# Kernel tuning notes

Hardware: AMD Instinct MI355X
Metric: run time of the kernel (lower is better)

Reference implementation:

```python
import jax, jax.numpy as jnp
import numpy as np

GAMMA = 2.0
NUM_CLASSES = 33

def _cdist(x):
    # pairwise euclidean distance per batch: x [B,N,C] -> [B,N,N]
    sq = jnp.sum(x * x, axis=-1)                      # [B,N]
    d2 = sq[:, :, None] + sq[:, None, :] - 2.0 * jnp.einsum('bnc,bmc->bnm', x, x)
    d2 = jnp.maximum(d2, 0.0)
    d = jnp.sqrt(jnp.where(d2 > 0, d2, 1.0))          # safe sqrt (zero-distance -> 0, no nan grad)
    return jnp.where(d2 > 0, d, 0.0)


def setup_inputs() -> dict:
    key = jax.random.key(0)
    k1, k2, k3 = jax.random.split(key, 3)
    B, N, C = 2, 4096, NUM_CLASSES
    predictions = jax.random.normal(k1, (B, N, C), dtype=jnp.float32)
    targets = jax.random.randint(k2, (B, N), 0, C, dtype=jnp.int32)
    y_ohe = jax.nn.one_hot(targets, C, dtype=jnp.float32)
    pred_choice = jax.random.randint(k3, (B, N), 0, C, dtype=jnp.int32)
    return {"predictions": predictions, "y_ohe": y_ohe, "targets": targets, "pred_choice": pred_choice}


def reference(predictions, y_ohe, targets, pred_choice):
    B, N, C = predictions.shape
    # cross-entropy (mean over all B*N positions, no class weights)
    logp = jax.nn.log_softmax(predictions, axis=-1)                       # [B,N,C]
    logp_t = jnp.take_along_axis(logp, targets[..., None].astype(jnp.int32), axis=-1)[..., 0]
    ce_loss = -jnp.mean(logp_t)                                           # scalar

    # distance-map KL term
    dis_map = _cdist(y_ohe)                                               # [B,N,N]
    dis_map = jnp.where(dis_map > 1.0, 0.9, dis_map)
    dis_map = jnp.where(dis_map < 1.0, 0.05, dis_map)
    pred_prob = jax.nn.softmax(predictions, axis=-1)
    pred_map = _cdist(pred_prob)                                          # [B,N,N]
    # torch F.kl_div(input, target) with default 'mean': mean(target*(log(target)-input))
    dis_map_loss = jnp.mean(dis_map * (jnp.log(dis_map) - pred_map))

    # focal weighting of the (scalar) CE loss
    pn = jnp.take_along_axis(jnp.exp(logp), targets[..., None].astype(jnp.int32), axis=-1)[..., 0]
    pn = pn.reshape(-1)                                                   # [B*N]
    loss = jnp.mean((1.0 - pn) ** GAMMA * ce_loss)

    # dice loss: per-class loop collapses exactly to a global match count
    eps = 1.0
    matches = jnp.sum((targets.reshape(-1) == pred_choice.reshape(-1)).astype(jnp.float32))
    total = targets.size
    dice = 1.0 - 2.0 * ((matches + eps) / (2.0 * total + eps))

    return loss + dice + dis_map_loss
```

## Files before the change

kernel.cpp:

```cpp
#include <hip/hip_runtime.h>
#include <math.h>

#define BB 2
#define NN 4096
#define CC 33
#define RP 40
#define TILE 64
#define NTILES (NN / TILE)
#define NJT 3
#define NPB 715
#define ROWBLK 256
#define PAIRBLK (BB * NPB)
#define NSLOT 64
#define SLOTSTR 32

#define AS1 __attribute__((address_space(1)))
#define AS3 __attribute__((address_space(3)))

typedef __attribute__((ext_vector_type(8))) short frag_ab;
typedef __attribute__((ext_vector_type(4))) float f32x4;

__device__ __forceinline__ float fast_sqrt(float x) {
    return __builtin_amdgcn_sqrtf(x);
}
__device__ __forceinline__ unsigned f2bf(float x) {
    unsigned u = __float_as_uint(x);
    return (u + 0x7FFFu + ((u >> 16) & 1u)) >> 16;
}
__device__ __forceinline__ float bf2f(unsigned b) {
    return __uint_as_float(b << 16);
}

__global__ __launch_bounds__(256) void row_kernel(
    const float* __restrict__ pred, const int* __restrict__ targets,
    const int* __restrict__ pred_choice, unsigned short* __restrict__ p16,
    float2* __restrict__ part_row, int* __restrict__ part_match,
    float* __restrict__ slotf, unsigned* __restrict__ subcnt,
    unsigned* __restrict__ master)
{
    __shared__ __align__(16) float sraw[32 * CC];
    __shared__ float2 lds_cf[4];
    __shared__ int lds_mt[4];

    if (blockIdx.x == 0) {
        for (int i = threadIdx.x; i < NSLOT * SLOTSTR; i += 256) {
            slotf[i] = 0.0f;
            subcnt[i] = 0u;
        }
        if (threadIdx.x == 0) *master = 0u;
    }

    int l = threadIdx.x & 63;
    int w = threadIdx.x >> 6;

    {
        const float4* src = (const float4*)(pred + (size_t)blockIdx.x * 32 * CC);
        __builtin_amdgcn_global_load_lds(
            (const AS1 void*)(src + w * 64 + l),
            (AS3 void*)((char*)sraw + w * 1024), 16, 0, 0);
        if (threadIdx.x < 8) {
            float4 tv = src[256 + threadIdx.x];
            ((float4*)sraw)[256 + threadIdx.x] = tv;
        }
    }
    __syncthreads();

    int r = l >> 3;
    int c = l & 7;
    int rloc = w * 8 + r;
    int row = blockIdx.x * 32 + rloc;

    float v[4];
    #pragma unroll
    for (int k = 0; k < 4; k++) v[k] = sraw[rloc * CC + 4 * c + k];
    float v32 = sraw[rloc * CC + 32];

    float m = fmaxf(fmaxf(v[0], v[1]), fmaxf(v[2], v[3]));
    if (c == 0) m = fmaxf(m, v32);
    m = fmaxf(m, __shfl_xor(m, 1));
    m = fmaxf(m, __shfl_xor(m, 2));
    m = fmaxf(m, __shfl_xor(m, 4));

    float e[4];
    float s = 0.0f;
    #pragma unroll
    for (int k = 0; k < 4; k++) { e[k] = __expf(v[k] - m); s += e[k]; }
    float e32 = __expf(v32 - m);
    if (c == 0) s += e32;
    s += __shfl_xor(s, 1);
    s += __shfl_xor(s, 2);
    s += __shfl_xor(s, 4);
    float inv = 1.0f / s;

    unsigned pb[4];
    float sq = 0.0f;
    #pragma unroll
    for (int k = 0; k < 4; k++) {
        pb[k] = f2bf(e[k] * inv);
        float pf = bf2f(pb[k]);
        sq += pf * pf;
    }
    unsigned c32u = f2bf(e32 * inv);
    float c32 = bf2f(c32u);
    if (c == 0) sq += c32 * c32;
    sq += __shfl_xor(sq, 1);
    sq += __shfl_xor(sq, 2);
    sq += __shfl_xor(sq, 4);

    {
        uint2 st = make_uint2(pb[0] | (pb[1] << 16), pb[2] | (pb[3] << 16));
        *(uint2*)&p16[(size_t)row * RP + 4 * c] = st;
    }
    if (c == 0) {
        uint4 st = make_uint4(c32u, __float_as_uint(sq), 0u, 0u);
        *(uint4*)&p16[(size_t)row * RP + 32] = st;
    }

    int tg = targets[row];
    float cand = 0.0f;
    if (tg < 32) {
        int cc = tg >> 2, kk = tg & 3;
        if (cc == c) cand = e[kk];
    } else if (c == 0) cand = e32;
    cand += __shfl_xor(cand, 1);
    cand += __shfl_xor(cand, 2);
    cand += __shfl_xor(cand, 4);

    float ce = 0.0f, fo = 0.0f; int mt = 0;
    if (c == 0) {
        float pt = cand * inv;
        ce = -__logf(pt);
        float om = 1.0f - pt;
        fo = om * om;
        mt = (tg == pred_choice[row]) ? 1 : 0;
    }
    ce += __shfl_xor(ce, 8);  ce += __shfl_xor(ce, 16);  ce += __shfl_xor(ce, 32);
    fo += __shfl_xor(fo, 8);  fo += __shfl_xor(fo, 16);  fo += __shfl_xor(fo, 32);
    mt += __shfl_xor(mt, 8);  mt += __shfl_xor(mt, 16);  mt += __shfl_xor(mt, 32);

    if (l == 0) { lds_cf[w] = make_float2(ce, fo); lds_mt[w] = mt; }
    __syncthreads();
    if (threadIdx.x == 0) {
        float2 a = lds_cf[0], b2 = lds_cf[1], c2 = lds_cf[2], d = lds_cf[3];
        part_row[blockIdx.x] = make_float2(a.x + b2.x + c2.x + d.x,
                                           a.y + b2.y + c2.y + d.y);
        part_match[blockIdx.x] = lds_mt[0] + lds_mt[1] + lds_mt[2] + lds_mt[3];
    }
}

__global__ __launch_bounds__(256) void pair_kernel(
    const unsigned short* __restrict__ p16,
    const float2* __restrict__ part_row, const int* __restrict__ part_match,
    float* __restrict__ slotf, unsigned* __restrict__ subcnt,
    unsigned* __restrict__ master, float* __restrict__ out)
{
    __shared__ __align__(16) unsigned short spj[NJT * TILE * RP];
    __shared__ float red[4];
    __shared__ int lastFlag;
    __shared__ double lds_ce[4], lds_fo[4], lds_pr[4];
    __shared__ int lds_mt[4];

    int bid = blockIdx.x;
    int b = bid / NPB;
    int t = bid % NPB;

    int ti = 0, rem = t;
    while (rem >= (NTILES - ti + NJT - 1) / NJT) {
        rem -= (NTILES - ti + NJT - 1) / NJT; ++ti;
    }
    int tjA = ti + NJT * rem;
    int avail = NTILES - tjA; if (avail > NJT) avail = NJT;
    bool diagA = (tjA == ti);
    int i0 = ti * TILE, j0A = tjA * TILE;

    int l = threadIdx.x & 63;
    int w = threadIdx.x >> 6;
    int col = l & 15;
    int kc = l >> 4;

    const unsigned short* pb16 = p16 + (size_t)b * NN * RP;

    {
        const float4* srcj = (const float4*)(pb16 + (size_t)j0A * RP);
        int nchunk = avail * 5;
        for (int c = w; c < nchunk; c += 4) {
            const float4* g = srcj + c * 64 + l;
            __builtin_amdgcn_global_load_lds(
                (const AS1 void*)g,
                (AS3 void*)((char*)spj + c * 1024),
                16, 0, 0);
        }
    }

    int arow = i0 + 16 * w + col;
    frag_ab afr = *(const frag_ab*)&pb16[(size_t)arow * RP + kc * 8];

    float qi[4], c32a[4];
    #pragma unroll
    for (int r = 0; r < 4; r++) {
        int ir = i0 + 16 * w + kc * 4 + r;
        uint2 md = *(const uint2*)&pb16[(size_t)ir * RP + 32];
        c32a[r] = bf2f(md.x);
        qi[r]   = __uint_as_float(md.y);
    }
    int gi0 = i0 + 16 * w + kc * 4;

    __syncthreads();

    float ssum = 0.0f;

    #pragma unroll
    for (int jt = 0; jt < NJT; jt++) {
        if (jt >= avail) break;
        const unsigned short* spjx = spj + jt * TILE * RP;
        int j0 = j0A + jt * TILE;
        bool dg = (jt == 0) && diagA;

        #pragma unroll
        for (int n = 0; n < 4; n++) {
            int jr = 16 * n + col;
            frag_ab bfr = *(const frag_ab*)&spjx[jr * RP + kc * 8];
            f32x4 acc = {0.0f, 0.0f, 0.0f, 0.0f};
            acc = __builtin_amdgcn_mfma_f32_16x16x32_bf16(afr, bfr, acc, 0, 0, 0);

            uint2 md = *(const uint2*)&spjx[jr * RP + 32];
            float c32b = bf2f(md.x);
            float qj   = __uint_as_float(md.y);
            int   gj   = j0 + 16 * n + col;

            #pragma unroll
            for (int r = 0; r < 4; r++) {
                float g  = fmaf(c32a[r], c32b, acc[r]);
                float d2 = fmaf(-2.0f, g, qi[r] + qj);
                float d  = fast_sqrt(fmaxf(d2, 0.0f));
                ssum += (!dg || gj > gi0 + r) ? d : 0.0f;
            }
        }
    }

    #pragma unroll
    for (int off = 32; off; off >>= 1) ssum += __shfl_xor(ssum, off);
    if (l == 0) red[w] = ssum;
    __syncthreads();

    if (threadIdx.x == 0) {
        float blockSum = red[0] + red[1] + red[2] + red[3];
        int slotIdx = bid & (NSLOT - 1);
        int slot = slotIdx * SLOTSTR;
        unsigned expect = (unsigned)(PAIRBLK / NSLOT) + (slotIdx < (PAIRBLK % NSLOT) ? 1u : 0u);
        __hip_atomic_fetch_add(&slotf[slot], blockSum,
                               __ATOMIC_RELAXED, __HIP_MEMORY_SCOPE_AGENT);
        asm volatile("s_waitcnt vmcnt(0)" ::: "memory");
        unsigned o = __hip_atomic_fetch_add(&subcnt[slot], 1u,
                                            __ATOMIC_RELAXED, __HIP_MEMORY_SCOPE_AGENT);
        int last = 0;
        if (o == expect - 1) {
            unsigned o2 = __hip_atomic_fetch_add(master, 1u,
                                                 __ATOMIC_RELAXED, __HIP_MEMORY_SCOPE_AGENT);
            last = (o2 == NSLOT - 1);
        }
        lastFlag = last;
    }
    __syncthreads();
    if (!lastFlag) return;

    double ce = 0.0, fo = 0.0, pr = 0.0;
    int mt = 0;
    for (int i = threadIdx.x; i < ROWBLK; i += 256) {
        float2 v = part_row[i];
        ce += (double)v.x;
        fo += (double)v.y;
        mt += part_match[i];
    }
    for (int i = threadIdx.x; i < NSLOT; i += 256)
        pr += (double)__hip_atomic_load(&slotf[i * SLOTSTR],
                                        __ATOMIC_RELAXED, __HIP_MEMORY_SCOPE_AGENT);

    #pragma unroll
    for (int off = 32; off; off >>= 1) {
        ce += __shfl_xor(ce, off);
        fo += __shfl_xor(fo, off);
        pr += __shfl_xor(pr, off);
        mt += __shfl_xor(mt, off);
    }
    if (l == 0) { lds_ce[w] = ce; lds_fo[w] = fo; lds_pr[w] = pr; lds_mt[w] = mt; }
    __syncthreads();
    if (threadIdx.x == 0) {
        double tce = lds_ce[0] + lds_ce[1] + lds_ce[2] + lds_ce[3];
        double tfo = lds_fo[0] + lds_fo[1] + lds_fo[2] + lds_fo[3];
        double tpr = lds_pr[0] + lds_pr[1] + lds_pr[2] + lds_pr[3];
        int    tmt = lds_mt[0] + lds_mt[1] + lds_mt[2] + lds_mt[3];

        double BN = (double)(BB * NN);
        double loss = (tce / BN) * (tfo / BN);
        double dice = 1.0 - 2.0 * ((double)tmt + 1.0) / (2.0 * BN + 1.0);
        double S = 2.0 * tpr;
        double mean_pred = S / (BN * (double)NN);
        double dml = 0.05 * log(0.05) - 0.05 * mean_pred;
        out[0] = (float)(loss + dice + dml);
    }
}

extern "C" void kernel_launch(void* const* d_in, const int* in_sizes, int n_in,
                              void* d_out, int out_size, void* d_ws, size_t ws_size,
                              hipStream_t stream)
{
    const float* pred        = (const float*)d_in[0];
    const int*   targets     = (const int*)d_in[2];
    const int*   pred_choice = (const int*)d_in[3];

    char* ws = (char*)d_ws;
    size_t off = 0;
    unsigned short* p16 = (unsigned short*)ws;
    off += (size_t)BB * NN * RP * sizeof(unsigned short);
    off = (off + 127) & ~(size_t)127;
    float2* part_row = (float2*)(ws + off);
    off += (size_t)ROWBLK * sizeof(float2);
    int* part_match = (int*)(ws + off);
    off += (size_t)ROWBLK * sizeof(int);
    off = (off + 127) & ~(size_t)127;
    float* slotf = (float*)(ws + off);
    off += (size_t)NSLOT * SLOTSTR * sizeof(float);
    unsigned* subcnt = (unsigned*)(ws + off);
    off += (size_t)NSLOT * SLOTSTR * sizeof(unsigned);
    unsigned* master = (unsigned*)(ws + off);
    off += sizeof(unsigned);

    row_kernel<<<ROWBLK, 256, 0, stream>>>(pred, targets, pred_choice,
                                           p16, part_row, part_match,
                                           slotf, subcnt, master);
    pair_kernel<<<PAIRBLK, 256, 0, stream>>>(p16, part_row, part_match,
                                             slotf, subcnt, master, (float*)d_out);
}
```

Baseline: 19.41 us.

## Fuse row and pair kernels with a grid-wide software barrier

Merges the row softmax kernel and the pairwise distance kernel into one launch. The first 256 blocks do the row work, then every block joins a two-level atomic counter barrier and spins on a go flag before the pair phase. Counters are now zeroed with a hipMemsetAsync instead of inside the row kernel. This removes the gap between the two kernel launches, but it relies on all 1430 blocks being co-resident (launch bounds request 6 blocks per CU) to avoid deadlock, and it adds a memset node plus spin-wait cost.

After: 23.26 us. 19.8% more time.

```diff
diff --git a/kernel.cpp b/kernel.cpp
--- a/kernel.cpp
+++ b/kernel.cpp
@@ -9,8 +9,8 @@
 #define NTILES (NN / TILE)
 #define NJT 3
 #define NPB 715
-#define ROWBLK 256
 #define PAIRBLK (BB * NPB)
+#define NROWBLK 256
 #define NSLOT 64
 #define SLOTSTR 32
 
@@ -19,6 +19,7 @@
 
 typedef __attribute__((ext_vector_type(8))) short frag_ab;
 typedef __attribute__((ext_vector_type(4))) float f32x4;
+typedef unsigned long long ull;
 
 __device__ __forceinline__ float fast_sqrt(float x) {
     return __builtin_amdgcn_sqrtf(x);
@@ -31,139 +32,131 @@
     return __uint_as_float(b << 16);
 }
 
-__global__ __launch_bounds__(256) void row_kernel(
+__global__ __launch_bounds__(256, 6) void fused_kernel(
     const float* __restrict__ pred, const int* __restrict__ targets,
     const int* __restrict__ pred_choice, unsigned short* __restrict__ p16,
     float2* __restrict__ part_row, int* __restrict__ part_match,
     float* __restrict__ slotf, unsigned* __restrict__ subcnt,
-    unsigned* __restrict__ master)
+    unsigned* __restrict__ master, unsigned* __restrict__ barr_sub,
+    unsigned* __restrict__ barr_master, unsigned* __restrict__ go,
+    float* __restrict__ out)
 {
-    __shared__ __align__(16) float sraw[32 * CC];
+    __shared__ __align__(16) unsigned short spj[NJT * TILE * RP];
+    __shared__ float red[4];
     __shared__ float2 lds_cf[4];
     __shared__ int lds_mt[4];
-
-    if (blockIdx.x == 0) {
-        for (int i = threadIdx.x; i < NSLOT * SLOTSTR; i += 256) {
-            slotf[i] = 0.0f;
-            subcnt[i] = 0u;
-        }
-        if (threadIdx.x == 0) *master = 0u;
-    }
-
+    __shared__ int lastFlag;
+    __shared__ double lds_ce[4], lds_fo[4], lds_pr[4];
+    __shared__ int lds_mt2[4];
+
+    int bid = blockIdx.x;
     int l = threadIdx.x & 63;
     int w = threadIdx.x >> 6;
 
-    {
-        const float4* src = (const float4*)(pred + (size_t)blockIdx.x * 32 * CC);
+    if (bid < NROWBLK) {
+        float* sraw = (float*)spj;
+        const float4* src = (const float4*)(pred + (size_t)bid * 32 * CC);
         __builtin_amdgcn_global_load_lds(
             (const AS1 void*)(src + w * 64 + l),
             (AS3 void*)((char*)sraw + w * 1024), 16, 0, 0);
-        if (threadIdx.x < 8) {
-            float4 tv = src[256 + threadIdx.x];
-            ((float4*)sraw)[256 + threadIdx.x] = tv;
-        }
-    }
-    __syncthreads();
-
-    int r = l >> 3;
-    int c = l & 7;
-    int rloc = w * 8 + r;
-    int row = blockIdx.x * 32 + rloc;
-
-    float v[4];
-    #pragma unroll
-    for (int k = 0; k < 4; k++) v[k] = sraw[rloc * CC + 4 * c + k];
-    float v32 = sraw[rloc * CC + 32];
-
-    float m = fmaxf(fmaxf(v[0], v[1]), fmaxf(v[2], v[3]));
-    if (c == 0) m = fmaxf(m, v32);
-    m = fmaxf(m, __shfl_xor(m, 1));
-    m = fmaxf(m, __shfl_xor(m, 2));
-    m = fmaxf(m, __shfl_xor(m, 4));
-
-    float e[4];
-    float s = 0.0f;
-    #pragma unroll
-    for (int k = 0; k < 4; k++) { e[k] = __expf(v[k] - m); s += e[k]; }
-    float e32 = __expf(v32 - m);
-    if (c == 0) s += e32;
-    s += __shfl_xor(s, 1);
-    s += __shfl_xor(s, 2);
-    s += __shfl_xor(s, 4);
-    float inv = 1.0f / s;
-
-    unsigned pb[4];
-    float sq = 0.0f;
-    #pragma unroll
-    for (int k = 0; k < 4; k++) {
-        pb[k] = f2bf(e[k] * inv);
-        float pf = bf2f(pb[k]);
-        sq += pf * pf;
-    }
-    unsigned c32u = f2bf(e32 * inv);
-    float c32 = bf2f(c32u);
-    if (c == 0) sq += c32 * c32;
-    sq += __shfl_xor(sq, 1);
-    sq += __shfl_xor(sq, 2);
-    sq += __shfl_xor(sq, 4);
-
-    {
-        uint2 st = make_uint2(pb[0] | (pb[1] << 16), pb[2] | (pb[3] << 16));
-        *(uint2*)&p16[(size_t)row * RP + 4 * c] = st;
-    }
-    if (c == 0) {
-        uint4 st = make_uint4(c32u, __float_as_uint(sq), 0u, 0u);
-        *(uint4*)&p16[(size_t)row * RP + 32] = st;
-    }
-
-    int tg = targets[row];
-    float cand = 0.0f;
-    if (tg < 32) {
-        int cc = tg >> 2, kk = tg & 3;
-        if (cc == c) cand = e[kk];
-    } else if (c == 0) cand = e32;
-    cand += __shfl_xor(cand, 1);
-    cand += __shfl_xor(cand, 2);
-    cand += __shfl_xor(cand, 4);
-
-    float ce = 0.0f, fo = 0.0f; int mt = 0;
-    if (c == 0) {
-        float pt = cand * inv;
-        ce = -__logf(pt);
-        float om = 1.0f - pt;
-        fo = om * om;
-        mt = (tg == pred_choice[row]) ? 1 : 0;
-    }
-    ce += __shfl_xor(ce, 8);  ce += __shfl_xor(ce, 16);  ce += __shfl_xor(ce, 32);
-    fo += __shfl_xor(fo, 8);  fo += __shfl_xor(fo, 16);  fo += __shfl_xor(fo, 32);
-    mt += __shfl_xor(mt, 8);  mt += __shfl_xor(mt, 16);  mt += __shfl_xor(mt, 32);
-
-    if (l == 0) { lds_cf[w] = make_float2(ce, fo); lds_mt[w] = mt; }
-    __syncthreads();
-    if (threadIdx.x == 0) {
-        float2 a = lds_cf[0], b2 = lds_cf[1], c2 = lds_cf[2], d = lds_cf[3];
-        part_row[blockIdx.x] = make_float2(a.x + b2.x + c2.x + d.x,
-                                           a.y + b2.y + c2.y + d.y);
-        part_match[blockIdx.x] = lds_mt[0] + lds_mt[1] + lds_mt[2] + lds_mt[3];
-    }
-}
-
-__global__ __launch_bounds__(256) void pair_kernel(
-    const unsigned short* __restrict__ p16,
-    const float2* __restrict__ part_row, const int* __restrict__ part_match,
-    float* __restrict__ slotf, unsigned* __restrict__ subcnt,
-    unsigned* __restrict__ master, float* __restrict__ out)
-{
-    __shared__ __align__(16) unsigned short spj[NJT * TILE * RP];
-    __shared__ float red[4];
-    __shared__ int lastFlag;
-    __shared__ double lds_ce[4], lds_fo[4], lds_pr[4];
-    __shared__ int lds_mt[4];
-
-    int bid = blockIdx.x;
+        if (threadIdx.x < 8)
+            ((float4*)sraw)[256 + threadIdx.x] = src[256 + threadIdx.x];
+        __syncthreads();
+
+        int r = l >> 3;
+        int c = l & 7;
+        int rloc = w * 8 + r;
+        int row = bid * 32 + rloc;
+
+        float v[4];
+        #pragma unroll
+        for (int k = 0; k < 4; k++) v[k] = sraw[rloc * CC + 4 * c + k];
+        float v32 = sraw[rloc * CC + 32];
+
+        float m = fmaxf(fmaxf(v[0], v[1]), fmaxf(v[2], v[3]));
+        if (c == 0) m = fmaxf(m, v32);
+        m = fmaxf(m, __shfl_xor(m, 1));
+        m = fmaxf(m, __shfl_xor(m, 2));
+        m = fmaxf(m, __shfl_xor(m, 4));
+
+        float e[4];
+        float s = 0.0f;
+        #pragma unroll
+        for (int k = 0; k < 4; k++) { e[k] = __expf(v[k] - m); s += e[k]; }
+        float e32 = __expf(v32 - m);
+        if (c == 0) s += e32;
+        s += __shfl_xor(s, 1);
+        s += __shfl_xor(s, 2);
+        s += __shfl_xor(s, 4);
+        float inv = 1.0f / s;
+
+        unsigned pb[4];
+        float sq = 0.0f;
+        #pragma unroll
+        for (int k = 0; k < 4; k++) {
+            pb[k] = f2bf(e[k] * inv);
+            float pf = bf2f(pb[k]);
+            sq += pf * pf;
+        }
+        unsigned c32u = f2bf(e32 * inv);
+        float c32 = bf2f(c32u);
+        if (c == 0) sq += c32 * c32;
+        sq += __shfl_xor(sq, 1);
+        sq += __shfl_xor(sq, 2);
+        sq += __shfl_xor(sq, 4);
+
+        ull pk = ((ull)(unsigned)(pb[2] | (pb[3] << 16)) << 32)
+               | (unsigned)(pb[0] | (pb[1] << 16));
+        __hip_atomic_store((ull*)&p16[(size_t)row * RP + 4 * c], pk,
+                           __ATOMIC_RELAXED, __HIP_MEMORY_SCOPE_AGENT);
+        if (c == 0) {
+            ull md = ((ull)__float_as_uint(sq) << 32) | (ull)c32u;
+            __hip_atomic_store((ull*)&p16[(size_t)row * RP + 32], md,
+                               __ATOMIC_RELAXED, __HIP_MEMORY_SCOPE_AGENT);
+            __hip_atomic_store((ull*)&p16[(size_t)row * RP + 36], 0ull,
+                               __ATOMIC_RELAXED, __HIP_MEMORY_SCOPE_AGENT);
+        }
+
+        int tg = targets[row];
+        float cand = 0.0f;
+        if (tg < 32) {
+            int cc = tg >> 2, kk = tg & 3;
+            if (cc == c) cand = e[kk];
+        } else if (c == 0) cand = e32;
+        cand += __shfl_xor(cand, 1);
+        cand += __shfl_xor(cand, 2);
+        cand += __shfl_xor(cand, 4);
+
+        float ce = 0.0f, fo = 0.0f; int mt = 0;
+        if (c == 0) {
+            float pt = cand * inv;
+            ce = -__logf(pt);
+            float om = 1.0f - pt;
+            fo = om * om;
+            mt = (tg == pred_choice[row]) ? 1 : 0;
+        }
+        ce += __shfl_xor(ce, 8);  ce += __shfl_xor(ce, 16);  ce += __shfl_xor(ce, 32);
+        fo += __shfl_xor(fo, 8);  fo += __shfl_xor(fo, 16);  fo += __shfl_xor(fo, 32);
+        mt += __shfl_xor(mt, 8);  mt += __shfl_xor(mt, 16);  mt += __shfl_xor(mt, 32);
+
+        if (l == 0) { lds_cf[w] = make_float2(ce, fo); lds_mt[w] = mt; }
+        __syncthreads();
+        if (threadIdx.x == 0) {
+            float2 a = lds_cf[0], b2 = lds_cf[1], c2 = lds_cf[2], d = lds_cf[3];
+            float ceS = a.x + b2.x + c2.x + d.x;
+            float foS = a.y + b2.y + c2.y + d.y;
+            int mtS = lds_mt[0] + lds_mt[1] + lds_mt[2] + lds_mt[3];
+            ull prw = ((ull)__float_as_uint(foS) << 32) | (ull)__float_as_uint(ceS);
+            __hip_atomic_store((ull*)&part_row[bid], prw,
+                               __ATOMIC_RELAXED, __HIP_MEMORY_SCOPE_AGENT);
+            __hip_atomic_store((unsigned*)&part_match[bid], (unsigned)mtS,
+                               __ATOMIC_RELAXED, __HIP_MEMORY_SCOPE_AGENT);
+        }
+        __syncthreads();
+    }
+
     int b = bid / NPB;
     int t = bid % NPB;
-
     int ti = 0, rem = t;
     while (rem >= (NTILES - ti + NJT - 1) / NJT) {
         rem -= (NTILES - ti + NJT - 1) / NJT; ++ti;
@@ -173,8 +166,25 @@
     bool diagA = (tjA == ti);
     int i0 = ti * TILE, j0A = tjA * TILE;
 
-    int l = threadIdx.x & 63;
-    int w = threadIdx.x >> 6;
+    if (threadIdx.x == 0) {
+        asm volatile("s_waitcnt vmcnt(0)" ::: "memory");
+        int slotIdx = bid & (NSLOT - 1);
+        unsigned bexp = (unsigned)(PAIRBLK / NSLOT)
+                      + (slotIdx < (PAIRBLK % NSLOT) ? 1u : 0u);
+        unsigned o = __hip_atomic_fetch_add(&barr_sub[slotIdx * SLOTSTR], 1u,
+                                            __ATOMIC_RELAXED, __HIP_MEMORY_SCOPE_AGENT);
+        if (o == bexp - 1) {
+            unsigned o2 = __hip_atomic_fetch_add(barr_master, 1u,
+                                                 __ATOMIC_RELAXED, __HIP_MEMORY_SCOPE_AGENT);
+            if (o2 == NSLOT - 1)
+                __hip_atomic_store(go, 1u, __ATOMIC_RELEASE, __HIP_MEMORY_SCOPE_AGENT);
+        }
+        while (__hip_atomic_load(go, __ATOMIC_RELAXED, __HIP_MEMORY_SCOPE_AGENT) == 0u)
+            __builtin_amdgcn_s_sleep(2);
+        asm volatile("" ::: "memory");
+    }
+    __syncthreads();
+
     int col = l & 15;
     int kc = l >> 4;
 
@@ -183,11 +193,11 @@
     {
         const float4* srcj = (const float4*)(pb16 + (size_t)j0A * RP);
         int nchunk = avail * 5;
-        for (int c = w; c < nchunk; c += 4) {
-            const float4* g = srcj + c * 64 + l;
+        for (int c2 = w; c2 < nchunk; c2 += 4) {
+            const float4* g = srcj + c2 * 64 + l;
             __builtin_amdgcn_global_load_lds(
                 (const AS1 void*)g,
-                (AS3 void*)((char*)spj + c * 1024),
+                (AS3 void*)((char*)spj + c2 * 1024),
                 16, 0, 0);
         }
     }
@@ -247,7 +257,8 @@
         float blockSum = red[0] + red[1] + red[2] + red[3];
         int slotIdx = bid & (NSLOT - 1);
         int slot = slotIdx * SLOTSTR;
-        unsigned expect = (unsigned)(PAIRBLK / NSLOT) + (slotIdx < (PAIRBLK % NSLOT) ? 1u : 0u);
+        unsigned expect = (unsigned)(PAIRBLK / NSLOT)
+                        + (slotIdx < (PAIRBLK % NSLOT) ? 1u : 0u);
         __hip_atomic_fetch_add(&slotf[slot], blockSum,
                                __ATOMIC_RELAXED, __HIP_MEMORY_SCOPE_AGENT);
         asm volatile("s_waitcnt vmcnt(0)" ::: "memory");
@@ -266,11 +277,13 @@
 
     double ce = 0.0, fo = 0.0, pr = 0.0;
     int mt = 0;
-    for (int i = threadIdx.x; i < ROWBLK; i += 256) {
-        float2 v = part_row[i];
-        ce += (double)v.x;
-        fo += (double)v.y;
-        mt += part_match[i];
+    for (int i = threadIdx.x; i < NROWBLK; i += 256) {
+        ull prw = __hip_atomic_load((const ull*)&part_row[i],
+                                    __ATOMIC_RELAXED, __HIP_MEMORY_SCOPE_AGENT);
+        ce += (double)__uint_as_float((unsigned)prw);
+        fo += (double)__uint_as_float((unsigned)(prw >> 32));
+        mt += (int)__hip_atomic_load((const unsigned*)&part_match[i],
+                                     __ATOMIC_RELAXED, __HIP_MEMORY_SCOPE_AGENT);
     }
     for (int i = threadIdx.x; i < NSLOT; i += 256)
         pr += (double)__hip_atomic_load(&slotf[i * SLOTSTR],
@@ -283,13 +296,13 @@
         pr += __shfl_xor(pr, off);
         mt += __shfl_xor(mt, off);
     }
-    if (l == 0) { lds_ce[w] = ce; lds_fo[w] = fo; lds_pr[w] = pr; lds_mt[w] = mt; }
+    if (l == 0) { lds_ce[w] = ce; lds_fo[w] = fo; lds_pr[w] = pr; lds_mt2[w] = mt; }
     __syncthreads();
     if (threadIdx.x == 0) {
         double tce = lds_ce[0] + lds_ce[1] + lds_ce[2] + lds_ce[3];
         double tfo = lds_fo[0] + lds_fo[1] + lds_fo[2] + lds_fo[3];
         double tpr = lds_pr[0] + lds_pr[1] + lds_pr[2] + lds_pr[3];
-        int    tmt = lds_mt[0] + lds_mt[1] + lds_mt[2] + lds_mt[3];
+        int    tmt = lds_mt2[0] + lds_mt2[1] + lds_mt2[2] + lds_mt2[3];
 
         double BN = (double)(BB * NN);
         double loss = (tce / BN) * (tfo / BN);
@@ -315,20 +328,30 @@
     off += (size_t)BB * NN * RP * sizeof(unsigned short);
     off = (off + 127) & ~(size_t)127;
     float2* part_row = (float2*)(ws + off);
-    off += (size_t)ROWBLK * sizeof(float2);
+    off += (size_t)NROWBLK * sizeof(float2);
     int* part_match = (int*)(ws + off);
-    off += (size_t)ROWBLK * sizeof(int);
+    off += (size_t)NROWBLK * sizeof(int);
     off = (off + 127) & ~(size_t)127;
+
+    char* sync_base = ws + off;
     float* slotf = (float*)(ws + off);
     off += (size_t)NSLOT * SLOTSTR * sizeof(float);
     unsigned* subcnt = (unsigned*)(ws + off);
     off += (size_t)NSLOT * SLOTSTR * sizeof(unsigned);
+    unsigned* barr_sub = (unsigned*)(ws + off);
+    off += (size_t)NSLOT * SLOTSTR * sizeof(unsigned);
+    unsigned* barr_master = (unsigned*)(ws + off);
+    off += 128;
+    unsigned* go = (unsigned*)(ws + off);
+    off += 128;
     unsigned* master = (unsigned*)(ws + off);
-    off += sizeof(unsigned);
-
-    row_kernel<<<ROWBLK, 256, 0, stream>>>(pred, targets, pred_choice,
-                                           p16, part_row, part_match,
-                                           slotf, subcnt, master);
-    pair_kernel<<<PAIRBLK, 256, 0, stream>>>(p16, part_row, part_match,
-                                             slotf, subcnt, master, (float*)d_out);
-}
+    off += 128;
+    size_t sync_bytes = (size_t)((ws + off) - sync_base);
+
+    hipMemsetAsync(sync_base, 0, sync_bytes, stream);
+    fused_kernel<<<PAIRBLK, 256, 0, stream>>>(pred, targets, pred_choice,
+                                              p16, part_row, part_match,
+                                              slotf, subcnt, master,
+                                              barr_sub, barr_master, go,
+                                              (float*)d_out);
+}
```
